# Kernel tuning notes

Hardware: AMD Instinct MI355X
Metric: run time of the kernel (lower is better)

Reference implementation:

```python
import jax, jax.numpy as jnp
import numpy as np

D_MODEL = 1024
NUM_HEADS = 16
HDIM = D_MODEL // NUM_HEADS
THETA = 10000.0


def setup_inputs() -> dict:
    key = jax.random.key(0)
    ks = jax.random.split(key, 5)
    bs, seq = 4, 2048
    std = np.sqrt(2.0 / (D_MODEL + D_MODEL))
    def w(k):
        # trunc_normal approximated by clipped normal (same distribution family)
        return jnp.clip(std * jax.random.normal(k, (D_MODEL, D_MODEL), jnp.float32), -3 * std, 3 * std)
    return {
        "x": jax.random.normal(ks[0], (bs, seq, D_MODEL), jnp.float32),
        "Wq": w(ks[1]), "Wk": w(ks[2]), "Wv": w(ks[3]), "Wo": w(ks[4]),
        "token_positions": jnp.arange(seq, dtype=jnp.int64),
    }


def _rope(x, token_positions):
    # x: (bs, H, S, hdim); rotate even/odd interleaved pairs
    inv_freq = THETA ** (-2.0 * jnp.arange(HDIM // 2, dtype=jnp.float32) / HDIM)
    freqs = token_positions.astype(jnp.float32)[:, None] * inv_freq[None, :]  # (S, hdim/2)
    cos, sin = jnp.cos(freqs), jnp.sin(freqs)
    x_even, x_odd = x[..., 0::2], x[..., 1::2]
    out_even = x_even * cos - x_odd * sin
    out_odd = x_odd * cos + x_even * sin
    # interleave back: stack on new last axis then reshape
    return jnp.stack([out_even, out_odd], axis=-1).reshape(x.shape)


def reference(x, Wq, Wk, Wv, Wo, token_positions):
    bs, seq, _ = x.shape
    q = (x @ Wq.T).reshape(bs, seq, NUM_HEADS, HDIM).transpose(0, 2, 1, 3)
    k = (x @ Wk.T).reshape(bs, seq, NUM_HEADS, HDIM).transpose(0, 2, 1, 3)
    v = (x @ Wv.T).reshape(bs, seq, NUM_HEADS, HDIM).transpose(0, 2, 1, 3)
    q = _rope(q, token_positions)
    k = _rope(k, token_positions)
    scores = jnp.einsum("bhsd,bhtd->bhst", q, k) / jnp.sqrt(jnp.float32(HDIM))
    mask = jnp.tril(jnp.ones((seq, seq), dtype=bool))
    scores = jnp.where(mask, scores, -jnp.inf)
    attn = jax.nn.softmax(scores, axis=-1)
    out = jnp.einsum("bhst,bhtd->bhsd", attn, v)
    out = out.transpose(0, 2, 1, 3).reshape(bs, seq, D_MODEL)
    return out @ Wo.T
```

## Files before the change

### kernel.cpp

```cpp
#include <hip/hip_runtime.h>
#include <hip/hip_fp16.h>

typedef _Float16 half8 __attribute__((ext_vector_type(8)));
typedef _Float16 half4 __attribute__((ext_vector_type(4)));
typedef _Float16 half2v __attribute__((ext_vector_type(2)));
typedef float f32x4 __attribute__((ext_vector_type(4)));
typedef float f32x8v __attribute__((ext_vector_type(8)));
typedef float f32x16 __attribute__((ext_vector_type(16)));

#define SEQ   2048
#define DM    1024
#define NH    16
#define HD    64
#define BSZ   4

#if __has_builtin(__builtin_amdgcn_exp2f)
#define EXP2(x) __builtin_amdgcn_exp2f(x)
#else
#define EXP2(x) exp2f(x)
#endif

#define QSCALE 0.1803368801f

__device__ __forceinline__ void gload16(const void* g, void* l) {
  __builtin_amdgcn_global_load_lds((const __attribute__((address_space(1))) void*)g,
                                   (__attribute__((address_space(3))) void*)l,
                                   16, 0, 0);
}

__global__ void cvt4(const float* __restrict__ src, _Float16* __restrict__ dst, int n4) {
  int i = blockIdx.x * blockDim.x + threadIdx.x;
  if (i < n4) {
    float4 v = ((const float4*)src)[i];
    half4 o = { (_Float16)v.x, (_Float16)v.y, (_Float16)v.z, (_Float16)v.w };
    ((half4*)dst)[i] = o;
  }
}

template<int MODE>
__global__ __launch_bounds__(256)
void gemm_hk(const _Float16* __restrict__ A, const _Float16* __restrict__ B,
             _Float16* __restrict__ oQ, _Float16* __restrict__ oK,
             _Float16* __restrict__ oVt, float* __restrict__ oF) {
  __shared__ _Float16 As[128*32];
  __shared__ _Float16 Bs[128*32];
  const int tid  = threadIdx.x;
  const int wid  = tid >> 6, lane = tid & 63;
  const int wm   = wid >> 1, wn = wid & 1;
  const int fr   = lane & 15, fg = lane >> 4;
  const long m0  = (long)blockIdx.x * 128;
  const long n0  = (long)blockIdx.y * 128;
  const int lrow = lane >> 2;
  const int lcol = (lane & 3) * 8;
  const _Float16* ga0 = A + (m0 + wid*32 + lrow) * 1024 + lcol;
  const _Float16* gb0 = B + (n0 + wid*32 + lrow) * 1024 + lcol;
  _Float16* lA = &As[wid*32*32];
  _Float16* lB = &Bs[wid*32*32];

  f32x4 acc[4][4] = {};

  for (int k0 = 0; k0 < 1024; k0 += 32) {
    gload16(ga0 + k0,             lA);
    gload16(ga0 + k0 + 16*1024,   lA + 16*32);
    gload16(gb0 + k0,             lB);
    gload16(gb0 + k0 + 16*1024,   lB + 16*32);
    __syncthreads();
    half8 af[4], bf[4];
#pragma unroll
    for (int i = 0; i < 4; ++i) {
      af[i] = *(const half8*)&As[(wm*64 + i*16 + fr)*32 + fg*8];
      bf[i] = *(const half8*)&Bs[(wn*64 + i*16 + fr)*32 + fg*8];
    }
#pragma unroll
    for (int i = 0; i < 4; ++i)
#pragma unroll
      for (int j = 0; j < 4; ++j)
        acc[i][j] = __builtin_amdgcn_mfma_f32_16x16x32_f16(af[i], bf[j], acc[i][j], 0, 0, 0);
    __syncthreads();
  }

  if (MODE == 0) {
    const int which = (int)(n0 >> 10);
    const int nloc0 = ((int)n0 & 1023) + wn*64;
#pragma unroll
    for (int i = 0; i < 4; ++i) {
      const long r0 = m0 + wm*64 + i*16 + fg*4;
      const int  bb = (int)(r0 >> 11);
      const int  s  = (int)(r0 & 2047);
#pragma unroll
      for (int j = 0; j < 4; ++j) {
        const int nl = nloc0 + j*16 + fr;
        const int h  = nl >> 6, d = nl & 63;
        const long bh = (long)(bb*NH + h);
        if (which == 0) {
#pragma unroll
          for (int r = 0; r < 4; ++r)
            oQ[(bh*SEQ + s + r)*HD + d] = (_Float16)(acc[i][j][r] * QSCALE);
        } else if (which == 1) {
#pragma unroll
          for (int r = 0; r < 4; ++r)
            oK[(bh*SEQ + s + r)*HD + d] = (_Float16)acc[i][j][r];
        } else {
          half4 pk = { (_Float16)acc[i][j][0], (_Float16)acc[i][j][1],
                       (_Float16)acc[i][j][2], (_Float16)acc[i][j][3] };
          *(half4*)&oVt[(bh*HD + d)*SEQ + s] = pk;
        }
      }
    }
  } else {
#pragma unroll
    for (int i = 0; i < 4; ++i) {
      const long r0 = m0 + wm*64 + i*16 + fg*4;
#pragma unroll
      for (int j = 0; j < 4; ++j) {
        const long col = n0 + wn*64 + j*16 + fr;
#pragma unroll
        for (int r = 0; r < 4; ++r)
          oF[(r0 + r)*DM + col] = acc[i][j][r];
      }
    }
  }
}

__global__ void rope_k(_Float16* __restrict__ Q, _Float16* __restrict__ K,
                       const int* __restrict__ tp) {
  const int t = blockIdx.x * blockDim.x + threadIdx.x;
  const int s = t >> 5, p = t & 31;
  _Float16* base = blockIdx.z ? K : Q;
  half2v* ptr = (half2v*)(base + ((long)blockIdx.y * SEQ + s) * HD) + p;
  half2v v = *ptr;
  const float pos = (float)tp[s];
  const float inv = exp2f(-0.41524101186f * (float)p);
  const float f = pos * inv;
  float sn, cs;
  __sincosf(f, &sn, &cs);
  const float xe = (float)v[0], xo = (float)v[1];
  half2v o = { (_Float16)(xe*cs - xo*sn), (_Float16)(xo*cs + xe*sn) };
  *ptr = o;
}

__global__ __launch_bounds__(256, 2)
void fattn(const _Float16* __restrict__ Q, const _Float16* __restrict__ K,
           const _Float16* __restrict__ Vt, _Float16* __restrict__ O) {
  __shared__ _Float16 Ks[2][64*64];
  __shared__ _Float16 Vs[2][64*64];
  __shared__ _Float16 Ps[4][32*64];
  const int tid = threadIdx.x, wid = tid >> 6, lane = tid & 63;
  const int q31 = lane & 31, hi = lane >> 5;
  const int bh = blockIdx.x, b = bh >> 4, h = bh & 15;
  const int y = blockIdx.y;
  const int qs_[2] = { (15 - y)*128 + wid*32, y*128 + wid*32 };
  const _Float16* Qb = Q + (long)bh * SEQ * HD;
  const _Float16* Kb = K + (long)bh * SEQ * HD;
  const _Float16* Vb = Vt + (long)bh * HD * SEQ;

  half8 qf[2][4];
#pragma unroll
  for (int s = 0; s < 2; ++s)
#pragma unroll
    for (int c = 0; c < 4; ++c)
      qf[s][c] = *(const half8*)&Qb[(qs_[s] + q31)*HD + c*16 + hi*8];

  f32x16 oacc[2][2] = {};
  float m_s[2] = { -1e30f, -1e30f }, l_s[2] = { 0.f, 0.f };

  const int srow = lane >> 3;
  const int sc16 = (lane & 7) ^ srow;
  const int r1 = wid*16 + srow, r2 = r1 + 8;

  char* Pb = (char*)&Ps[wid][0];
  const int swp = (q31 & 7) << 4;
  const int nt = (15 - y)*2 + 2;

  gload16(Kb + (long)r1*HD + sc16*8, &Ks[0][(wid*16)*64]);
  gload16(Kb + (long)r2*HD + sc16*8, &Ks[0][(wid*16 + 8)*64]);
  gload16(Vb + (long)r1*SEQ + sc16*8, &Vs[0][(wid*16)*64]);
  gload16(Vb + (long)r2*SEQ + sc16*8, &Vs[0][(wid*16 + 8)*64]);
  __syncthreads();

  int cur = 0;
  for (int t = 0; t < nt; ++t) {
    const int kv0 = t * 64;

    if (t + 1 < nt) {
      const int nkv = kv0 + 64;
      gload16(Kb + (long)(nkv + r1)*HD + sc16*8, &Ks[cur^1][(wid*16)*64]);
      gload16(Kb + (long)(nkv + r2)*HD + sc16*8, &Ks[cur^1][(wid*16 + 8)*64]);
      gload16(Vb + (long)r1*SEQ + nkv + sc16*8,  &Vs[cur^1][(wid*16)*64]);
      gload16(Vb + (long)r2*SEQ + nkv + sc16*8,  &Vs[cur^1][(wid*16 + 8)*64]);
    }

    const char* Kc = (const char*)&Ks[cur][0];
    const char* Vc = (const char*)&Vs[cur][0];

#pragma unroll
    for (int hh = 0; hh < 2; ++hh) {
      const int kvb = kv0 + 32*hh;
#pragma unroll
      for (int s = 0; s < 2; ++s) {
        const int qs0 = qs_[s];
        if (kvb > qs0 + 31) continue;

        f32x16 sa = {};
        __builtin_amdgcn_s_setprio(1);
#pragma unroll
        for (int c = 0; c < 4; ++c) {
          const int row = 32*hh + q31;
          const half8 kf = *(const half8*)(Kc + row*128 + ((c*32 + hi*16) ^ ((row & 7) << 4)));
          sa = __builtin_amdgcn_mfma_f32_32x32x16_f16(kf, qf[s][c], sa, 0, 0, 0);
        }
        __builtin_amdgcn_s_setprio(0);

        if (kvb + 31 > qs0) {
          const int thr = qs0 + q31 - kvb - 4*hi;
#pragma unroll
          for (int r = 0; r < 16; ++r) {
            const int cr = (r & 3) + 8*(r >> 2);
            if (cr > thr) sa[r] = -1e30f;
          }
        }

        f32x8v mx8;
#pragma unroll
        for (int i = 0; i < 8; ++i) mx8[i] = fmaxf(sa[i], sa[i+8]);
        f32x4 mx4;
#pragma unroll
        for (int i = 0; i < 4; ++i) mx4[i] = fmaxf(mx8[i], mx8[i+4]);
        float pm = fmaxf(fmaxf(mx4[0], mx4[1]), fmaxf(mx4[2], mx4[3]));
        pm = fmaxf(pm, __shfl_xor(pm, 32));

        if (!__all(pm <= m_s[s] + 8.0f)) {
          const float mn = fmaxf(m_s[s], pm);
          const float fac = EXP2(m_s[s] - mn);
          m_s[s] = mn;
          l_s[s] *= fac;
          oacc[s][0] *= fac;
          oacc[s][1] *= fac;
        }
        const float mrow = m_s[s];

#pragma unroll
        for (int r = 0; r < 16; ++r) sa[r] = EXP2(sa[r] - mrow);

        f32x8v s8;
#pragma unroll
        for (int i = 0; i < 8; ++i) s8[i] = sa[i] + sa[i+8];
        f32x4 s4v;
#pragma unroll
        for (int i = 0; i < 4; ++i) s4v[i] = s8[i] + s8[i+4];
        float ps = (s4v[0] + s4v[1]) + (s4v[2] + s4v[3]);
        ps += __shfl_xor(ps, 32);
        l_s[s] += ps;

#pragma unroll
        for (int g = 0; g < 4; ++g) {
          half2v lo  = (half2v)__builtin_amdgcn_cvt_pkrtz(sa[4*g+0], sa[4*g+1]);
          half2v hi2 = (half2v)__builtin_amdgcn_cvt_pkrtz(sa[4*g+2], sa[4*g+3]);
          half4 p4 = __builtin_shufflevector(lo, hi2, 0, 1, 2, 3);
          *(half4*)(Pb + q31*128 + ((g*16 + hi*8) ^ swp)) = p4;
        }

        __builtin_amdgcn_s_setprio(1);
#pragma unroll
        for (int ks = 0; ks < 2; ++ks) {
          const half8 pf = *(const half8*)(Pb + q31*128 + ((ks*32 + hi*16) ^ swp));
#pragma unroll
          for (int nd = 0; nd < 2; ++nd) {
            const int row = nd*32 + q31;
            const half8 vf = *(const half8*)(Vc + row*128 +
                              ((hh*64 + ks*32 + hi*16) ^ ((row & 7) << 4)));
            oacc[s][nd] = __builtin_amdgcn_mfma_f32_32x32x16_f16(vf, pf, oacc[s][nd], 0, 0, 0);
          }
        }
        __builtin_amdgcn_s_setprio(0);
      }
    }

    __syncthreads();
    cur ^= 1;
  }

#pragma unroll
  for (int s = 0; s < 2; ++s) {
    const float rl = __builtin_amdgcn_rcpf(l_s[s]);
    _Float16* orow = O + ((long)b*SEQ + (qs_[s] + q31))*DM + h*64;
#pragma unroll
    for (int nd = 0; nd < 2; ++nd)
#pragma unroll
      for (int g = 0; g < 4; ++g) {
        half2v lo  = (half2v)__builtin_amdgcn_cvt_pkrtz(oacc[s][nd][4*g+0]*rl, oacc[s][nd][4*g+1]*rl);
        half2v hi2 = (half2v)__builtin_amdgcn_cvt_pkrtz(oacc[s][nd][4*g+2]*rl, oacc[s][nd][4*g+3]*rl);
        half4 o4 = __builtin_shufflevector(lo, hi2, 0, 1, 2, 3);
        *(half4*)&orow[nd*32 + g*8 + 4*hi] = o4;
      }
  }
}

extern "C" void kernel_launch(void* const* d_in, const int* in_sizes, int n_in,
                              void* d_out, int out_size, void* d_ws, size_t ws_size,
                              hipStream_t stream) {
  const float* x  = (const float*)d_in[0];
  const float* Wq = (const float*)d_in[1];
  const float* Wk = (const float*)d_in[2];
  const float* Wv = (const float*)d_in[3];
  const float* Wo = (const float*)d_in[4];
  const int*   tp = (const int*)d_in[5];
  float* out = (float*)d_out;

  char* ws = (char*)d_ws;
  _Float16* xh   = (_Float16*)(ws);
  _Float16* Wqkv = (_Float16*)(ws + (16u << 20));
  _Float16* Woh  = (_Float16*)(ws + (22u << 20));
  _Float16* Qb   = (_Float16*)(ws + (24u << 20));
  _Float16* Kb   = (_Float16*)(ws + (40u << 20));
  _Float16* Vtb  = (_Float16*)(ws + (56u << 20));
  _Float16* attn = (_Float16*)(ws + (72u << 20));

  cvt4<<<8192, 256, 0, stream>>>(x,  xh, 2097152);
  cvt4<<<1024, 256, 0, stream>>>(Wq, Wqkv,               262144);
  cvt4<<<1024, 256, 0, stream>>>(Wk, Wqkv + (1u << 20),  262144);
  cvt4<<<1024, 256, 0, stream>>>(Wv, Wqkv + (2u << 20),  262144);
  cvt4<<<1024, 256, 0, stream>>>(Wo, Woh,                262144);

  gemm_hk<0><<<dim3(64, 24), 256, 0, stream>>>(xh, Wqkv, Qb, Kb, Vtb, nullptr);
  rope_k<<<dim3(256, 64, 2), 256, 0, stream>>>(Qb, Kb, tp);
  fattn<<<dim3(64, 8), 256, 0, stream>>>(Qb, Kb, Vtb, attn);
  gemm_hk<1><<<dim3(64, 8), 256, 0, stream>>>(attn, Woh, nullptr, nullptr, nullptr, out);
}
```

Baseline: 196.1 us.

## Fuse RoPE into QKV GEMM epilogue and double-buffer GEMM LDS tiles

Removes the standalone RoPE kernel by applying the rotation in the QKV GEMM epilogue. Each lane gets its even/odd partner through a lane shuffle and computes sin/cos from the token positions there. The GEMM main loop now double-buffers the A/B LDS tiles, prefetching the next K slice while MFMAs run, and raises wave priority around the MFMA block. This saves one kernel launch plus a read-modify-write pass over Q and K. In exchange it doubles LDS use per block and adds transcendental work to the epilogue.

```diff
diff --git a/kernel.cpp b/kernel.cpp
--- a/kernel.cpp
+++ b/kernel.cpp
@@ -21,6 +21,7 @@
 #endif
 
 #define QSCALE 0.1803368801f
+#define ROPE_C 0.41524101186f
 
 __device__ __forceinline__ void gload16(const void* g, void* l) {
   __builtin_amdgcn_global_load_lds((const __attribute__((address_space(1))) void*)g,
@@ -41,9 +42,10 @@
 __global__ __launch_bounds__(256)
 void gemm_hk(const _Float16* __restrict__ A, const _Float16* __restrict__ B,
              _Float16* __restrict__ oQ, _Float16* __restrict__ oK,
-             _Float16* __restrict__ oVt, float* __restrict__ oF) {
-  __shared__ _Float16 As[128*32];
-  __shared__ _Float16 Bs[128*32];
+             _Float16* __restrict__ oVt, float* __restrict__ oF,
+             const int* __restrict__ tp) {
+  __shared__ _Float16 As[2][128*32];
+  __shared__ _Float16 Bs[2][128*32];
   const int tid  = threadIdx.x;
   const int wid  = tid >> 6, lane = tid & 63;
   const int wm   = wid >> 1, wn = wid & 1;
@@ -54,34 +56,45 @@
   const int lcol = (lane & 3) * 8;
   const _Float16* ga0 = A + (m0 + wid*32 + lrow) * 1024 + lcol;
   const _Float16* gb0 = B + (n0 + wid*32 + lrow) * 1024 + lcol;
-  _Float16* lA = &As[wid*32*32];
-  _Float16* lB = &Bs[wid*32*32];
+  const int lofs = wid*32*32;
 
   f32x4 acc[4][4] = {};
 
+  gload16(ga0,           &As[0][lofs]);
+  gload16(ga0 + 16*1024, &As[0][lofs + 16*32]);
+  gload16(gb0,           &Bs[0][lofs]);
+  gload16(gb0 + 16*1024, &Bs[0][lofs + 16*32]);
+  __syncthreads();
+
+  int cur = 0;
   for (int k0 = 0; k0 < 1024; k0 += 32) {
-    gload16(ga0 + k0,             lA);
-    gload16(ga0 + k0 + 16*1024,   lA + 16*32);
-    gload16(gb0 + k0,             lB);
-    gload16(gb0 + k0 + 16*1024,   lB + 16*32);
-    __syncthreads();
+    if (k0 + 32 < 1024) {
+      gload16(ga0 + k0 + 32,           &As[cur^1][lofs]);
+      gload16(ga0 + k0 + 32 + 16*1024, &As[cur^1][lofs + 16*32]);
+      gload16(gb0 + k0 + 32,           &Bs[cur^1][lofs]);
+      gload16(gb0 + k0 + 32 + 16*1024, &Bs[cur^1][lofs + 16*32]);
+    }
     half8 af[4], bf[4];
 #pragma unroll
     for (int i = 0; i < 4; ++i) {
-      af[i] = *(const half8*)&As[(wm*64 + i*16 + fr)*32 + fg*8];
-      bf[i] = *(const half8*)&Bs[(wn*64 + i*16 + fr)*32 + fg*8];
-    }
+      af[i] = *(const half8*)&As[cur][(wm*64 + i*16 + fr)*32 + fg*8];
+      bf[i] = *(const half8*)&Bs[cur][(wn*64 + i*16 + fr)*32 + fg*8];
+    }
+    __builtin_amdgcn_s_setprio(1);
 #pragma unroll
     for (int i = 0; i < 4; ++i)
 #pragma unroll
       for (int j = 0; j < 4; ++j)
         acc[i][j] = __builtin_amdgcn_mfma_f32_16x16x32_f16(af[i], bf[j], acc[i][j], 0, 0, 0);
+    __builtin_amdgcn_s_setprio(0);
     __syncthreads();
+    cur ^= 1;
   }
 
   if (MODE == 0) {
     const int which = (int)(n0 >> 10);
     const int nloc0 = ((int)n0 & 1023) + wn*64;
+    const bool odd = fr & 1;
 #pragma unroll
     for (int i = 0; i < 4; ++i) {
       const long r0 = m0 + wm*64 + i*16 + fg*4;
@@ -92,18 +105,24 @@
         const int nl = nloc0 + j*16 + fr;
         const int h  = nl >> 6, d = nl & 63;
         const long bh = (long)(bb*NH + h);
-        if (which == 0) {
-#pragma unroll
-          for (int r = 0; r < 4; ++r)
-            oQ[(bh*SEQ + s + r)*HD + d] = (_Float16)(acc[i][j][r] * QSCALE);
-        } else if (which == 1) {
-#pragma unroll
-          for (int r = 0; r < 4; ++r)
-            oK[(bh*SEQ + s + r)*HD + d] = (_Float16)acc[i][j][r];
-        } else {
+        if (which == 2) {
           half4 pk = { (_Float16)acc[i][j][0], (_Float16)acc[i][j][1],
                        (_Float16)acc[i][j][2], (_Float16)acc[i][j][3] };
           *(half4*)&oVt[(bh*HD + d)*SEQ + s] = pk;
+        } else {
+          const float inv = exp2f(-ROPE_C * (float)(d >> 1));
+#pragma unroll
+          for (int r = 0; r < 4; ++r) {
+            const float v = acc[i][j][r];
+            const float p = __shfl_xor(v, 1);
+            float sn, cs;
+            __sincosf((float)tp[s + r] * inv, &sn, &cs);
+            const float out = odd ? (v*cs + p*sn) : (v*cs - p*sn);
+            if (which == 0)
+              oQ[(bh*SEQ + s + r)*HD + d] = (_Float16)(out * QSCALE);
+            else
+              oK[(bh*SEQ + s + r)*HD + d] = (_Float16)out;
+          }
         }
       }
     }
@@ -120,23 +139,6 @@
       }
     }
   }
-}
-
-__global__ void rope_k(_Float16* __restrict__ Q, _Float16* __restrict__ K,
-                       const int* __restrict__ tp) {
-  const int t = blockIdx.x * blockDim.x + threadIdx.x;
-  const int s = t >> 5, p = t & 31;
-  _Float16* base = blockIdx.z ? K : Q;
-  half2v* ptr = (half2v*)(base + ((long)blockIdx.y * SEQ + s) * HD) + p;
-  half2v v = *ptr;
-  const float pos = (float)tp[s];
-  const float inv = exp2f(-0.41524101186f * (float)p);
-  const float f = pos * inv;
-  float sn, cs;
-  __sincosf(f, &sn, &cs);
-  const float xe = (float)v[0], xo = (float)v[1];
-  half2v o = { (_Float16)(xe*cs - xo*sn), (_Float16)(xo*cs + xe*sn) };
-  *ptr = o;
 }
 
 __global__ __launch_bounds__(256, 2)
@@ -322,8 +324,7 @@
   cvt4<<<1024, 256, 0, stream>>>(Wv, Wqkv + (2u << 20),  262144);
   cvt4<<<1024, 256, 0, stream>>>(Wo, Woh,                262144);
 
-  gemm_hk<0><<<dim3(64, 24), 256, 0, stream>>>(xh, Wqkv, Qb, Kb, Vtb, nullptr);
-  rope_k<<<dim3(256, 64, 2), 256, 0, stream>>>(Qb, Kb, tp);
+  gemm_hk<0><<<dim3(64, 24), 256, 0, stream>>>(xh, Wqkv, Qb, Kb, Vtb, nullptr, tp);
   fattn<<<dim3(64, 8), 256, 0, stream>>>(Qb, Kb, Vtb, attn);
-  gemm_hk<1><<<dim3(64, 8), 256, 0, stream>>>(attn, Woh, nullptr, nullptr, nullptr, out);
-}
+  gemm_hk<1><<<dim3(64, 8), 256, 0, stream>>>(attn, Woh, nullptr, nullptr, nullptr, out, nullptr);
+}
```

After: 182.0 us. 1.08x faster.
